# Performance work log

Hardware: AMD Instinct MI355X
Metric: run time of the kernel (lower is better)

Reference implementation:

```python
import jax, jax.numpy as jnp
import numpy as np
import math

B, S, D = 2, 2048, 2048
H = 16
DK = D // H  # 128
DFF = 5440
THETA = 10000.0
EPS = 1e-5


def setup_inputs() -> dict:
    key = jax.random.key(0)
    ks = jax.random.split(key, 9)
    sc = 0.02
    return {
        "x": jax.random.normal(ks[0], (B, S, D), jnp.float32),
        "wq": jax.random.normal(ks[1], (D, D), jnp.float32) * sc,
        "wk": jax.random.normal(ks[2], (D, D), jnp.float32) * sc,
        "wv": jax.random.normal(ks[3], (D, D), jnp.float32) * sc,
        "wo": jax.random.normal(ks[4], (D, D), jnp.float32) * sc,
        "w1": jax.random.normal(ks[5], (DFF, D), jnp.float32) * sc,
        "w2": jax.random.normal(ks[6], (D, DFF), jnp.float32) * sc,
        "w3": jax.random.normal(ks[7], (DFF, D), jnp.float32) * sc,
        "g_attn": jnp.ones((D,), jnp.float32),
        "g_ffn": jnp.ones((D,), jnp.float32),
    }


def _rmsnorm(x, g):
    xf = x.astype(jnp.float32)
    rms = jnp.sqrt(jnp.mean(xf * xf, axis=-1, keepdims=True) + EPS)
    return (xf / rms * g).astype(x.dtype)


def _rope(x):
    # x: (B, H, S, DK)
    pair = jnp.arange(0, DK, 2, dtype=jnp.float32)
    inv_freq = 1.0 / (THETA ** (pair / DK))            # (DK/2,)
    pos = jnp.arange(S, dtype=jnp.float32)
    ang = pos[:, None] * inv_freq[None, :]             # (S, DK/2)
    cos, sin = jnp.cos(ang), jnp.sin(ang)
    xe, xo = x[..., 0::2], x[..., 1::2]
    oe = xe * cos - xo * sin
    oo = xe * sin + xo * cos
    # interleave even/odd back
    out = jnp.stack([oe, oo], axis=-1).reshape(x.shape)
    return out


def reference(x, wq, wk, wv, wo, w1, w2, w3, g_attn, g_ffn):
    # --- attention sublayer ---
    h = _rmsnorm(x, g_attn)
    q = (h @ wq.T).reshape(B, S, H, DK).transpose(0, 2, 1, 3)
    k = (h @ wk.T).reshape(B, S, H, DK).transpose(0, 2, 1, 3)
    v = (h @ wv.T).reshape(B, S, H, DK).transpose(0, 2, 1, 3)
    q = _rope(q)
    k = _rope(k)
    scores = jnp.einsum("bhqd,bhkd->bhqk", q, k) / math.sqrt(DK)
    causal = jnp.tril(jnp.ones((S, S), dtype=bool))
    scores = jnp.where(causal, scores, jnp.finfo(scores.dtype).min)
    attn = jax.nn.softmax(scores, axis=-1)
    o = jnp.einsum("bhqk,bhkd->bhqd", attn, v)
    o = o.transpose(0, 2, 1, 3).reshape(B, S, D)
    x = x + o @ wo.T
    # --- SwiGLU FFN sublayer ---
    h = _rmsnorm(x, g_ffn)
    a = h @ w1.T
    gate = a * jax.nn.sigmoid(a)
    ff = (gate * (h @ w3.T)) @ w2.T
    return x + ff
```

## Files before the change

kernel.cpp:

```cpp
#include <hip/hip_runtime.h>
#include <cstdint>
#include <cstddef>

typedef float  f32x4  __attribute__((ext_vector_type(4)));
typedef __bf16 bf16x8 __attribute__((ext_vector_type(8)));
typedef unsigned short u16x8 __attribute__((ext_vector_type(8)));
typedef unsigned short u16x4 __attribute__((ext_vector_type(4)));
typedef unsigned short u16x2 __attribute__((ext_vector_type(2)));

#define DEV static __device__ __forceinline__

DEV unsigned short f2bfu(float f) { __bf16 b = (__bf16)f; return __builtin_bit_cast(unsigned short, b); }
DEV float bfu2f(unsigned short u) { return (float)__builtin_bit_cast(__bf16, u); }
DEV bf16x8 ldb8(const void* p) { return __builtin_bit_cast(bf16x8, *(const u16x8*)p); }
DEV float fexp(float x) { return __builtin_amdgcn_exp2f(x * 1.44269504f); }

DEV f32x4 mfma16(bf16x8 a, bf16x8 b, f32x4 c) {
  return __builtin_amdgcn_mfma_f32_16x16x32_bf16(a, b, c, 0, 0, 0);
}

DEV void gload16(const void* g, void* l) {
  __builtin_amdgcn_global_load_lds((const unsigned int*)g, (unsigned int*)l, 16, 0, 0);
}

#define FENCE() asm volatile("" ::: "memory")
#define LGKM0() asm volatile("s_waitcnt lgkmcnt(0)" ::: "memory")
#define VMC4()  asm volatile("s_waitcnt vmcnt(4)" ::: "memory")
#define VMC0()  asm volatile("s_waitcnt vmcnt(0)" ::: "memory")

__global__ __launch_bounds__(256) void conv_cat3(
    const float* __restrict__ s0, const float* __restrict__ s1,
    const float* __restrict__ s2, unsigned short* __restrict__ d)
{
  size_t i = (size_t)blockIdx.x * 256 + threadIdx.x;
  size_t e = i * 4;
  const float* s = e < 4194304 ? s0 : (e < 8388608 ? s1 : s2);
  f32x4 v = *(const f32x4*)(s + (e & 4194303));
  u16x4 o = { f2bfu(v.x), f2bfu(v.y), f2bfu(v.z), f2bfu(v.w) };
  *(u16x4*)(d + e) = o;
}

__global__ __launch_bounds__(256) void conv_plain(
    const float* __restrict__ s, unsigned short* __restrict__ d)
{
  size_t e = ((size_t)blockIdx.x * 256 + threadIdx.x) * 4;
  f32x4 v = *(const f32x4*)(s + e);
  u16x4 o = { f2bfu(v.x), f2bfu(v.y), f2bfu(v.z), f2bfu(v.w) };
  *(u16x4*)(d + e) = o;
}

__global__ __launch_bounds__(256) void conv_w13(
    const float* __restrict__ w1, const float* __restrict__ w3,
    unsigned short* __restrict__ d)
{
  size_t i = (size_t)blockIdx.x * 256 + threadIdx.x;
  size_t e = i * 4;
  if (e >= 22544384ull) return;
  int n = (int)(e >> 11), kc = (int)(e & 2047);
  int grp = n >> 4;
  int srcrow = (grp >> 1) * 16 + (n & 15);
  if (srcrow >= 5440) srcrow = 5439;
  const float* s = (grp & 1) ? w3 : w1;
  size_t off = (size_t)srcrow * 2048 + kc;
  f32x4 v = *(const f32x4*)(s + off);
  u16x4 o = { f2bfu(v.x), f2bfu(v.y), f2bfu(v.z), f2bfu(v.w) };
  *(u16x4*)(d + e) = o;
}

template<int EPI>
__global__ __launch_bounds__(256) void gemm_f(
    const unsigned short* __restrict__ A, const unsigned short* __restrict__ B,
    void* __restrict__ D0, void* __restrict__ D1, void* __restrict__ D2,
    const float* __restrict__ auxf, const float* __restrict__ cosT,
    const float* __restrict__ sinT, int M, int N, int K)
{
  __shared__ __align__(16) unsigned short As[128 * 64];
  __shared__ __align__(16) unsigned short Bs[128 * 64];
  const int tid = threadIdx.x, lane = tid & 63, w = tid >> 6;
  const int wr = w >> 1, wc = w & 1, l15 = lane & 15, lg = lane >> 4;
  const int m0 = blockIdx.x * 128, n0 = blockIdx.y * 128;

  const int srow  = tid >> 3;
  const int scol8 = (tid & 7) ^ (srow & 7);
  const unsigned short* Asrc = A + (size_t)(m0 + srow) * K + scol8 * 8;
  const unsigned short* Bsrc = B + (size_t)(n0 + srow) * K + scol8 * 8;

  f32x4 zero = {0.f, 0.f, 0.f, 0.f};
  f32x4 acc[4][4];
#pragma unroll
  for (int i = 0; i < 4; i++)
#pragma unroll
    for (int j = 0; j < 4; j++) acc[i][j] = zero;

  for (int k0 = 0; k0 < K; k0 += 64) {
#pragma unroll
    for (int p = 0; p < 4; ++p) {
      gload16(Asrc + (size_t)(p * 32) * K + k0, As + (p * 256 + w * 64) * 8);
      gload16(Bsrc + (size_t)(p * 32) * K + k0, Bs + (p * 256 + w * 64) * 8);
    }
    __syncthreads();
    bf16x8 af[2][4], bfr[2][4];
#pragma unroll
    for (int kk = 0; kk < 2; ++kk) {
#pragma unroll
      for (int i = 0; i < 4; ++i) {
        int rA = wr * 64 + i * 16 + l15;
        af[kk][i]  = ldb8(As + rA * 64 + ((((kk << 2) | lg)) ^ (rA & 7)) * 8);
        int rB = wc * 64 + i * 16 + l15;
        bfr[kk][i] = ldb8(Bs + rB * 64 + ((((kk << 2) | lg)) ^ (rB & 7)) * 8);
      }
    }
#pragma unroll
    for (int kk = 0; kk < 2; ++kk)
#pragma unroll
      for (int mi = 0; mi < 4; mi++)
#pragma unroll
        for (int ni = 0; ni < 4; ni++)
          acc[mi][ni] = mfma16(af[kk][mi], bfr[kk][ni], acc[mi][ni]);
    __syncthreads();
  }

  if constexpr (EPI == 0) {
    unsigned short* qd = (unsigned short*)D0;
    unsigned short* kd = (unsigned short*)D1;
    unsigned short* vd = (unsigned short*)D2;
#pragma unroll
    for (int mi = 0; mi < 4; mi++) {
#pragma unroll
      for (int ni = 0; ni < 4; ni++) {
        int col = n0 + wc * 64 + ni * 16 + l15;
#pragma unroll
        for (int r = 0; r < 4; r++) {
          int row = m0 + wr * 64 + mi * 16 + lg * 4 + r;
          float v = acc[mi][ni][r];
          if (col < 4096) {
            int d = col & 127, pi = d >> 1, sp = row & 2047;
            float c = cosT[sp * 64 + pi], s = sinT[sp * 64 + pi];
            float part = __shfl_xor(v, 1);
            float res = (d & 1) ? (part * s + v * c) : (v * c - part * s);
            unsigned short* dst = (col < 2048) ? qd : kd;
            dst[(size_t)row * 2048 + (col & 2047)] = f2bfu(res);
          } else {
            int vdc = col - 4096;
            vd[((size_t)((row >> 11) * 2048 + vdc)) * 2048 + (row & 2047)] = f2bfu(v);
          }
        }
      }
    }
  } else {
    float* O = (float*)D0;
#pragma unroll
    for (int mi = 0; mi < 4; mi++)
#pragma unroll
      for (int ni = 0; ni < 4; ni++) {
        int col = n0 + wc * 64 + ni * 16 + l15;
#pragma unroll
        for (int r = 0; r < 4; r++) {
          int row = m0 + wr * 64 + mi * 16 + lg * 4 + r;
          size_t ix = (size_t)row * 2048 + col;
          if constexpr (EPI == 1) O[ix] = auxf[ix] + acc[mi][ni][r];
          else                    O[ix] = O[ix] + acc[mi][ni][r];
        }
      }
  }
}

template<int EPI>
__global__ __launch_bounds__(512, 1) void gemm8(
    const unsigned short* __restrict__ A, const unsigned short* __restrict__ B,
    void* __restrict__ D0, int M, int N, int K)
{
  __shared__ __align__(16) char Asb[3 * 16384];
  __shared__ __align__(16) char Bsb[3 * 16384];

  const int tid = threadIdx.x, lane = tid & 63, w = tid >> 6;
  const int wm = w >> 2, wn = w & 3;
  const int l15 = lane & 15, lg = lane >> 4;

  const int nwg = gridDim.x, chunk = nwg >> 3;
  const int wg = (blockIdx.x & 7) * chunk + (blockIdx.x >> 3);
  const int MT = M >> 8;
  const int mt = wg % MT, nt = wg / MT;
  const int m0 = mt * 256, n0 = nt * 256;

  const int srow0 = tid >> 2, srow1 = 128 + srow0;
  const int s4d = tid & 3;
  const int s4s0 = s4d ^ ((srow0 >> 1) & 3);
  const int s4s1 = s4d ^ ((srow1 >> 1) & 3);
  const size_t aoff0 = (size_t)(m0 + srow0) * K + s4s0 * 8;
  const size_t aoff1 = (size_t)(m0 + srow1) * K + s4s1 * 8;
  const size_t boff0 = (size_t)(n0 + srow0) * K + s4s0 * 8;
  const size_t boff1 = (size_t)(n0 + srow1) * K + s4s1 * 8;
  const int d0b = srow0 * 64 + s4d * 16;
  const int d1b = srow1 * 64 + s4d * 16;

  f32x4 zero = {0.f, 0.f, 0.f, 0.f};
  f32x4 acc[8][4];
#pragma unroll
  for (int i = 0; i < 8; i++)
#pragma unroll
    for (int j = 0; j < 4; j++) acc[i][j] = zero;

  const int nkt = K >> 5;

  gload16(A + aoff0, Asb + d0b);
  gload16(A + aoff1, Asb + d1b);
  gload16(B + boff0, Bsb + d0b);
  gload16(B + boff1, Bsb + d1b);
  gload16(A + aoff0 + 32, Asb + 16384 + d0b);
  gload16(A + aoff1 + 32, Asb + 16384 + d1b);
  gload16(B + boff0 + 32, Bsb + 16384 + d0b);
  gload16(B + boff1 + 32, Bsb + 16384 + d1b);
  VMC4();
  FENCE();
  __builtin_amdgcn_s_barrier();

  int arow[8], aro[8], brow[4], bro[4];
#pragma unroll
  for (int mi = 0; mi < 8; mi++) {
    arow[mi] = wm * 128 + mi * 16 + l15;
    aro[mi] = arow[mi] * 64 + ((lg ^ ((arow[mi] >> 1) & 3)) << 4);
  }
#pragma unroll
  for (int ni = 0; ni < 4; ni++) {
    brow[ni] = wn * 64 + ni * 16 + l15;
    bro[ni] = brow[ni] * 64 + ((lg ^ ((brow[ni] >> 1) & 3)) << 4);
  }

  int cur = 0, nxt = 2;
  for (int t = 0; t < nkt; ++t) {
    const char* As = Asb + cur * 16384;
    const char* Bs = Bsb + cur * 16384;
    const bool pf = (t + 2) < nkt;
    const size_t kpf = (size_t)(t + 2) * 32;
    char* Apf = Asb + nxt * 16384;
    char* Bpf = Bsb + nxt * 16384;

    bf16x8 bf_[4], af_[4];
#pragma unroll
    for (int ni = 0; ni < 4; ni++) bf_[ni] = ldb8(Bs + bro[ni]);
#pragma unroll
    for (int mi = 0; mi < 4; mi++) af_[mi] = ldb8(As + aro[mi]);
    if (pf) {
      gload16(A + aoff0 + kpf, Apf + d0b);
      gload16(A + aoff1 + kpf, Apf + d1b);
    }
    FENCE();
    __builtin_amdgcn_s_barrier();
    LGKM0();
    __builtin_amdgcn_sched_barrier(0);
    __builtin_amdgcn_s_setprio(1);
#pragma unroll
    for (int mi = 0; mi < 4; mi++)
#pragma unroll
      for (int ni = 0; ni < 4; ni++)
        acc[mi][ni] = mfma16(af_[mi], bf_[ni], acc[mi][ni]);
    __builtin_amdgcn_s_setprio(0);
    FENCE();
    __builtin_amdgcn_s_barrier();

    bf16x8 ag_[4];
#pragma unroll
    for (int mi = 0; mi < 4; mi++) ag_[mi] = ldb8(As + aro[mi + 4]);
    if (pf) {
      gload16(B + boff0 + kpf, Bpf + d0b);
      gload16(B + boff1 + kpf, Bpf + d1b);
    }
    FENCE();
    __builtin_amdgcn_s_barrier();
    LGKM0();
    __builtin_amdgcn_sched_barrier(0);
    __builtin_amdgcn_s_setprio(1);
#pragma unroll
    for (int mi = 0; mi < 4; mi++)
#pragma unroll
      for (int ni = 0; ni < 4; ni++)
        acc[mi + 4][ni] = mfma16(ag_[mi], bf_[ni], acc[mi + 4][ni]);
    __builtin_amdgcn_s_setprio(0);
    if (pf) { VMC4(); } else { VMC0(); }
    FENCE();
    __builtin_amdgcn_s_barrier();

    cur = cur == 2 ? 0 : cur + 1;
    nxt = nxt == 2 ? 0 : nxt + 1;
  }

  if constexpr (EPI == 2) {
    unsigned short* G = (unsigned short*)D0;
#pragma unroll
    for (int mi = 0; mi < 8; mi++)
#pragma unroll
      for (int nj = 0; nj < 2; nj++) {
        int outc = (nt * 8 + wn * 2 + nj) * 16 + l15;
        if (outc >= 5440) continue;
#pragma unroll
        for (int r = 0; r < 4; r++) {
          int row = m0 + wm * 128 + mi * 16 + lg * 4 + r;
          float a = acc[mi][2 * nj][r];
          float c = acc[mi][2 * nj + 1][r];
          float sg = a / (1.0f + fexp(-a));
          G[(size_t)row * 5440 + outc] = f2bfu(sg * c);
        }
      }
  }
}

__global__ __launch_bounds__(256) void rmsnorm_k(
    const float* __restrict__ x, const float* __restrict__ g,
    unsigned short* __restrict__ out)
{
  int row = blockIdx.x, t = threadIdx.x;
  const float* xr = x + (size_t)row * 2048;
  f32x4 v0 = ((const f32x4*)xr)[t];
  f32x4 v1 = ((const f32x4*)xr)[t + 256];
  float ss = v0.x*v0.x + v0.y*v0.y + v0.z*v0.z + v0.w*v0.w
           + v1.x*v1.x + v1.y*v1.y + v1.z*v1.z + v1.w*v1.w;
  __shared__ float red[256];
  red[t] = ss; __syncthreads();
  for (int sh = 128; sh > 0; sh >>= 1) {
    if (t < sh) red[t] += red[t + sh];
    __syncthreads();
  }
  float rinv = rsqrtf(red[0] * (1.0f / 2048.0f) + 1e-5f);
  f32x4 g0 = ((const f32x4*)g)[t];
  f32x4 g1 = ((const f32x4*)g)[t + 256];
  u16x4 o0 = { f2bfu(v0.x*rinv*g0.x), f2bfu(v0.y*rinv*g0.y),
               f2bfu(v0.z*rinv*g0.z), f2bfu(v0.w*rinv*g0.w) };
  u16x4 o1 = { f2bfu(v1.x*rinv*g1.x), f2bfu(v1.y*rinv*g1.y),
               f2bfu(v1.z*rinv*g1.z), f2bfu(v1.w*rinv*g1.w) };
  *(u16x4*)(out + (size_t)row * 2048 + t * 4) = o0;
  *(u16x4*)(out + (size_t)row * 2048 + 1024 + t * 4) = o1;
}

__global__ __launch_bounds__(256) void rope_tab(float* __restrict__ cosT,
                                                float* __restrict__ sinT)
{
  int idx = blockIdx.x * 256 + threadIdx.x;
  int s = idx >> 6, p = idx & 63;
  float ang = (float)s * powf(10000.0f, -(float)p / 64.0f);
  cosT[idx] = cosf(ang);
  sinT[idx] = sinf(ang);
}

__global__ __launch_bounds__(256) void attn_fwd(
    const unsigned short* __restrict__ q, const unsigned short* __restrict__ k,
    const unsigned short* __restrict__ vt, unsigned short* __restrict__ o)
{
  const int S = 2048, Dm = 2048;
  const int tid  = threadIdx.x;
  const int lane = tid & 63;
  const int w    = tid >> 6;
  const int hh   = blockIdx.y, b = blockIdx.z;
  const int l15  = lane & 15, lg = lane >> 4;
  const float SCALE = 0.08838834764831845f;

  __shared__ __align__(16) unsigned short Ks[64 * 128];
  __shared__ __align__(16) unsigned short Vs[128 * 64];
  __shared__ __align__(16) unsigned short Ps[4][16 * 76];

  const unsigned short* kg = k  + ((size_t)(b * S)) * Dm + hh * 128;
  const unsigned short* vg = vt + ((size_t)((b * 16 + hh) * 128)) * S;

  for (int half = 0; half < 2; ++half) {
    const int qt = half ? (31 - blockIdx.x) : blockIdx.x;
    const int r0 = qt * 64;
    const int myq = r0 + w * 16 + l15;

    bf16x8 qf[4];
    size_t qbase = ((size_t)(b * S + r0 + w * 16 + l15)) * Dm + hh * 128 + lg * 8;
#pragma unroll
    for (int kk = 0; kk < 4; kk++) qf[kk] = ldb8(q + qbase + kk * 32);

    f32x4 zero = {0.f, 0.f, 0.f, 0.f};
    f32x4 accO[8];
#pragma unroll
    for (int dt = 0; dt < 8; dt++) accO[dt] = zero;
    float mrun = -1e30f, lrun = 0.f;

    int ntile = qt + 1;
    for (int j = 0; j < ntile; ++j) {
      int kv0 = j * 64;
#pragma unroll
      for (int i = 0; i < 4; i++) {
        int idx = i * 256 + tid;
        int row = idx >> 4, slot = idx & 15;
        u16x8 vv = *(const u16x8*)(kg + (size_t)(kv0 + row) * Dm + slot * 8);
        int boff = (row * 256 + slot * 16) ^ ((row & 7) << 4);
        *(u16x8*)((char*)Ks + boff) = vv;
      }
#pragma unroll
      for (int i = 0; i < 4; i++) {
        int idx = i * 256 + tid;
        int row = idx >> 3, slot = idx & 7;
        u16x8 vv = *(const u16x8*)(vg + (size_t)row * S + kv0 + slot * 8);
        int boff = (row * 128 + slot * 16) ^ ((row & 7) << 4);
        *(u16x8*)((char*)Vs + boff) = vv;
      }
      __syncthreads();

      f32x4 sfr[4];
#pragma unroll
      for (int sv = 0; sv < 4; sv++) sfr[sv] = zero;
#pragma unroll
      for (int kk = 0; kk < 4; kk++) {
#pragma unroll
        for (int sv = 0; sv < 4; sv++) {
          int row = sv * 16 + l15;
          int boff = (row * 256 + kk * 64 + lg * 16) ^ ((row & 7) << 4);
          bf16x8 kf = ldb8((const unsigned short*)((const char*)Ks + boff));
          sfr[sv] = mfma16(kf, qf[kk], sfr[sv]);
        }
      }

      float tmax = -1e30f;
#pragma unroll
      for (int sv = 0; sv < 4; sv++)
#pragma unroll
        for (int r = 0; r < 4; r++) {
          int kvv = kv0 + sv * 16 + lg * 4 + r;
          float val = (kvv <= myq) ? sfr[sv][r] * SCALE : -1e30f;
          sfr[sv][r] = val;
          tmax = fmaxf(tmax, val);
        }
      tmax = fmaxf(tmax, __shfl_xor(tmax, 16));
      tmax = fmaxf(tmax, __shfl_xor(tmax, 32));
      float mnew = fmaxf(mrun, tmax);
      float alpha = fexp(mrun - mnew);
      float psum = 0.f;
#pragma unroll
      for (int sv = 0; sv < 4; sv++)
#pragma unroll
        for (int r = 0; r < 4; r++) {
          float pvv = fexp(sfr[sv][r] - mnew);
          sfr[sv][r] = pvv;
          psum += pvv;
        }
      psum += __shfl_xor(psum, 16);
      psum += __shfl_xor(psum, 32);
      lrun = lrun * alpha + psum;
      mrun = mnew;

      float al[4];
#pragma unroll
      for (int r = 0; r < 4; r++)
        al[r] = __shfl(alpha, (lane & 48) + lg * 4 + r);
#pragma unroll
      for (int dt = 0; dt < 8; dt++) {
        f32x4 t = accO[dt];
        t[0] *= al[0]; t[1] *= al[1]; t[2] *= al[2]; t[3] *= al[3];
        accO[dt] = t;
      }

#pragma unroll
      for (int sv = 0; sv < 4; sv++) {
        u16x2 lo = { f2bfu(sfr[sv][0]), f2bfu(sfr[sv][1]) };
        u16x2 hi = { f2bfu(sfr[sv][2]), f2bfu(sfr[sv][3]) };
        *(u16x2*)&Ps[w][l15 * 76 + sv * 16 + lg * 4]     = lo;
        *(u16x2*)&Ps[w][l15 * 76 + sv * 16 + lg * 4 + 2] = hi;
      }

      bf16x8 pa[2];
      pa[0] = ldb8(&Ps[w][l15 * 76 + lg * 8]);
      pa[1] = ldb8(&Ps[w][l15 * 76 + 32 + lg * 8]);
#pragma unroll
      for (int dt = 0; dt < 8; dt++) {
#pragma unroll
        for (int kk = 0; kk < 2; kk++) {
          int row = dt * 16 + l15;
          int boff = (row * 128 + kk * 64 + lg * 16) ^ ((row & 7) << 4);
          bf16x8 vb = ldb8((const unsigned short*)((const char*)Vs + boff));
          accO[dt] = mfma16(pa[kk], vb, accO[dt]);
        }
      }
      __syncthreads();
    }

    float lf[4];
#pragma unroll
    for (int r = 0; r < 4; r++)
      lf[r] = __shfl(lrun, (lane & 48) + lg * 4 + r);
#pragma unroll
    for (int dt = 0; dt < 8; dt++) {
#pragma unroll
      for (int r = 0; r < 4; r++) {
        int qr = r0 + w * 16 + lg * 4 + r;
        o[((size_t)(b * S + qr)) * Dm + hh * 128 + dt * 16 + l15] =
            f2bfu(accO[dt][r] / lf[r]);
      }
    }
  }
}

extern "C" void kernel_launch(void* const* d_in, const int* in_sizes, int n_in,
                              void* d_out, int out_size, void* d_ws, size_t ws_size,
                              hipStream_t stream)
{
  const float* x      = (const float*)d_in[0];
  const float* wq     = (const float*)d_in[1];
  const float* wk     = (const float*)d_in[2];
  const float* wv     = (const float*)d_in[3];
  const float* wo     = (const float*)d_in[4];
  const float* w1     = (const float*)d_in[5];
  const float* w2     = (const float*)d_in[6];
  const float* w3     = (const float*)d_in[7];
  const float* g_attn = (const float*)d_in[8];
  const float* g_ffn  = (const float*)d_in[9];
  float* out = (float*)d_out;

  unsigned short* W = (unsigned short*)d_ws;
  unsigned short* h_bf    = W;
  unsigned short* q_bf    = W + 8388608ull;
  unsigned short* k_bf    = W + 16777216ull;
  unsigned short* vt_bf   = W + 25165824ull;
  unsigned short* o_bf    = W + 33554432ull;
  unsigned short* wqkv_bf = W + 41943040ull;
  unsigned short* wo_bf   = W + 54525952ull;
  unsigned short* w13_bf  = W + 58720256ull;
  unsigned short* w2_bf   = W + 81264640ull;
  unsigned short* a1_bf   = q_bf;
  float* cosT = (float*)o_bf;
  float* sinT = cosT + 131072;

  dim3 blk(256);
  rope_tab<<<512, blk, 0, stream>>>(cosT, sinT);
  conv_cat3<<<12288, blk, 0, stream>>>(wq, wk, wv, wqkv_bf);
  conv_plain<<<4096, blk, 0, stream>>>(wo, wo_bf);
  conv_w13<<<22016, blk, 0, stream>>>(w1, w3, w13_bf);
  conv_plain<<<10880, blk, 0, stream>>>(w2, w2_bf);

  rmsnorm_k<<<4096, blk, 0, stream>>>(x, g_attn, h_bf);

  gemm_f<0><<<dim3(32, 48), blk, 0, stream>>>(h_bf, wqkv_bf, q_bf, k_bf, vt_bf,
                                              nullptr, cosT, sinT, 4096, 6144, 2048);

  attn_fwd<<<dim3(16, 16, 2), blk, 0, stream>>>(q_bf, k_bf, vt_bf, o_bf);

  gemm_f<1><<<dim3(32, 16), blk, 0, stream>>>(o_bf, wo_bf, out, nullptr, nullptr,
                                              x, nullptr, nullptr, 4096, 2048, 2048);
  rmsnorm_k<<<4096, blk, 0, stream>>>(out, g_ffn, h_bf);

  gemm8<2><<<dim3(688), dim3(512), 0, stream>>>(h_bf, w13_bf, a1_bf, 4096, 11008, 2048);

  gemm_f<3><<<dim3(32, 16), blk, 0, stream>>>(a1_bf, w2_bf, out, nullptr, nullptr,
                                              nullptr, nullptr, nullptr, 4096, 2048, 5440);
}
```

Baseline: 726.1 us.

## Double-buffer K-loop in gemm8 and async-prefetch KV tiles in attention

The SwiGLU GEMM now processes 64-wide K steps across two 32-wide half-stages that are double-buffered in 128KB of LDS, with fewer barriers per 32 elements of K. The attention kernel swaps synchronous global-to-register-to-LDS copies of K/V for direct global_load_lds prefetches into double-buffered shared memory, so the next tile loads while the current one is computed. This aims to hide global memory latency and remove register staging, at the cost of more LDS, which may reduce occupancy for attention, and more delicate vmcnt accounting.

New measurement: 698.1 us. 1.04x faster.

```diff
diff --git a/kernel.cpp b/kernel.cpp
--- a/kernel.cpp
+++ b/kernel.cpp
@@ -25,8 +25,13 @@
 
 #define FENCE() asm volatile("" ::: "memory")
 #define LGKM0() asm volatile("s_waitcnt lgkmcnt(0)" ::: "memory")
+#define VMC8()  asm volatile("s_waitcnt vmcnt(8)" ::: "memory")
 #define VMC4()  asm volatile("s_waitcnt vmcnt(4)" ::: "memory")
 #define VMC0()  asm volatile("s_waitcnt vmcnt(0)" ::: "memory")
+#define SBAR()  __builtin_amdgcn_s_barrier()
+#define SCH0()  __builtin_amdgcn_sched_barrier(0)
+#define PRIO1() __builtin_amdgcn_s_setprio(1)
+#define PRIO0() __builtin_amdgcn_s_setprio(0)
 
 __global__ __launch_bounds__(256) void conv_cat3(
     const float* __restrict__ s0, const float* __restrict__ s1,
@@ -166,12 +171,12 @@
 }
 
 template<int EPI>
-__global__ __launch_bounds__(512, 1) void gemm8(
+__global__ __launch_bounds__(512, 1) void gemm8v2(
     const unsigned short* __restrict__ A, const unsigned short* __restrict__ B,
     void* __restrict__ D0, int M, int N, int K)
 {
-  __shared__ __align__(16) char Asb[3 * 16384];
-  __shared__ __align__(16) char Bsb[3 * 16384];
+  __shared__ __align__(16) char Asb[4 * 16384];
+  __shared__ __align__(16) char Bsb[4 * 16384];
 
   const int tid = threadIdx.x, lane = tid & 63, w = tid >> 6;
   const int wm = w >> 2, wn = w & 3;
@@ -183,16 +188,21 @@
   const int mt = wg % MT, nt = wg / MT;
   const int m0 = mt * 256, n0 = nt * 256;
 
-  const int srow0 = tid >> 2, srow1 = 128 + srow0;
-  const int s4d = tid & 3;
-  const int s4s0 = s4d ^ ((srow0 >> 1) & 3);
-  const int s4s1 = s4d ^ ((srow1 >> 1) & 3);
-  const size_t aoff0 = (size_t)(m0 + srow0) * K + s4s0 * 8;
-  const size_t aoff1 = (size_t)(m0 + srow1) * K + s4s1 * 8;
-  const size_t boff0 = (size_t)(n0 + srow0) * K + s4s0 * 8;
-  const size_t boff1 = (size_t)(n0 + srow1) * K + s4s1 * 8;
-  const int d0b = srow0 * 64 + s4d * 16;
-  const int d1b = srow1 * 64 + s4d * 16;
+  const int srow = tid >> 2;
+  const int s4   = tid & 3;
+  const int s4s  = s4 ^ ((srow >> 1) & 3);
+  const unsigned short* As0 = A + (size_t)(m0 + srow) * K + s4s * 8;
+  const unsigned short* As1 = A + (size_t)(m0 + 128 + srow) * K + s4s * 8;
+  const unsigned short* Bs0 = B + (size_t)(n0 + srow) * K + s4s * 8;
+  const unsigned short* Bs1 = B + (size_t)(n0 + 128 + srow) * K + s4s * 8;
+  const int dst0 = tid * 16, dst1 = 8192 + tid * 16;
+
+#define STAGE_A(kh, db, kt) do { char* rgn = Asb + ((kh)*2+(db))*16384;       \
+    gload16(As0 + (size_t)(kt)*64 + (kh)*32, rgn + dst0);                      \
+    gload16(As1 + (size_t)(kt)*64 + (kh)*32, rgn + dst1); } while(0)
+#define STAGE_B(kh, db, kt) do { char* rgn = Bsb + ((kh)*2+(db))*16384;       \
+    gload16(Bs0 + (size_t)(kt)*64 + (kh)*32, rgn + dst0);                      \
+    gload16(Bs1 + (size_t)(kt)*64 + (kh)*32, rgn + dst1); } while(0)
 
   f32x4 zero = {0.f, 0.f, 0.f, 0.f};
   f32x4 acc[8][4];
@@ -201,89 +211,89 @@
 #pragma unroll
     for (int j = 0; j < 4; j++) acc[i][j] = zero;
 
-  const int nkt = K >> 5;
-
-  gload16(A + aoff0, Asb + d0b);
-  gload16(A + aoff1, Asb + d1b);
-  gload16(B + boff0, Bsb + d0b);
-  gload16(B + boff1, Bsb + d1b);
-  gload16(A + aoff0 + 32, Asb + 16384 + d0b);
-  gload16(A + aoff1 + 32, Asb + 16384 + d1b);
-  gload16(B + boff0 + 32, Bsb + 16384 + d0b);
-  gload16(B + boff1 + 32, Bsb + 16384 + d1b);
-  VMC4();
-  FENCE();
-  __builtin_amdgcn_s_barrier();
-
-  int arow[8], aro[8], brow[4], bro[4];
+  int aro[8], bro[4];
 #pragma unroll
   for (int mi = 0; mi < 8; mi++) {
-    arow[mi] = wm * 128 + mi * 16 + l15;
-    aro[mi] = arow[mi] * 64 + ((lg ^ ((arow[mi] >> 1) & 3)) << 4);
+    int row = wm * 128 + mi * 16 + l15;
+    aro[mi] = row * 64 + ((lg ^ ((row >> 1) & 3)) << 4);
   }
 #pragma unroll
   for (int ni = 0; ni < 4; ni++) {
-    brow[ni] = wn * 64 + ni * 16 + l15;
-    bro[ni] = brow[ni] * 64 + ((lg ^ ((brow[ni] >> 1) & 3)) << 4);
-  }
-
-  int cur = 0, nxt = 2;
+    int row = wn * 64 + ni * 16 + l15;
+    bro[ni] = row * 64 + ((lg ^ ((row >> 1) & 3)) << 4);
+  }
+
+  const int nkt = K >> 6;
+
+  STAGE_A(0, 0, 0); STAGE_B(0, 0, 0); STAGE_A(1, 0, 0); STAGE_B(1, 0, 0);
+
   for (int t = 0; t < nkt; ++t) {
-    const char* As = Asb + cur * 16384;
-    const char* Bs = Bsb + cur * 16384;
-    const bool pf = (t + 2) < nkt;
-    const size_t kpf = (size_t)(t + 2) * 32;
-    char* Apf = Asb + nxt * 16384;
-    char* Bpf = Bsb + nxt * 16384;
-
-    bf16x8 bf_[4], af_[4];
-#pragma unroll
-    for (int ni = 0; ni < 4; ni++) bf_[ni] = ldb8(Bs + bro[ni]);
-#pragma unroll
-    for (int mi = 0; mi < 4; mi++) af_[mi] = ldb8(As + aro[mi]);
-    if (pf) {
-      gload16(A + aoff0 + kpf, Apf + d0b);
-      gload16(A + aoff1 + kpf, Apf + d1b);
-    }
-    FENCE();
-    __builtin_amdgcn_s_barrier();
-    LGKM0();
-    __builtin_amdgcn_sched_barrier(0);
-    __builtin_amdgcn_s_setprio(1);
+    const int db = t & 1, dn = db ^ 1;
+    const bool pf = (t + 1) < nkt;
+    const char* Ar0 = Asb + (0 * 2 + db) * 16384;
+    const char* Br0 = Bsb + (0 * 2 + db) * 16384;
+    const char* Ar1 = Asb + (1 * 2 + db) * 16384;
+    const char* Br1 = Bsb + (1 * 2 + db) * 16384;
+
+    VMC4(); FENCE(); SBAR();
+    bf16x8 bfr[4], af[4];
+#pragma unroll
+    for (int ni = 0; ni < 4; ni++) bfr[ni] = ldb8(Br0 + bro[ni]);
+#pragma unroll
+    for (int mi = 0; mi < 4; mi++) af[mi] = ldb8(Ar0 + aro[mi]);
+    if (pf) STAGE_A(0, dn, t + 1);
+    LGKM0(); SCH0();
+    PRIO1();
 #pragma unroll
     for (int mi = 0; mi < 4; mi++)
 #pragma unroll
       for (int ni = 0; ni < 4; ni++)
-        acc[mi][ni] = mfma16(af_[mi], bf_[ni], acc[mi][ni]);
-    __builtin_amdgcn_s_setprio(0);
-    FENCE();
-    __builtin_amdgcn_s_barrier();
-
-    bf16x8 ag_[4];
-#pragma unroll
-    for (int mi = 0; mi < 4; mi++) ag_[mi] = ldb8(As + aro[mi + 4]);
-    if (pf) {
-      gload16(B + boff0 + kpf, Bpf + d0b);
-      gload16(B + boff1 + kpf, Bpf + d1b);
-    }
-    FENCE();
-    __builtin_amdgcn_s_barrier();
-    LGKM0();
-    __builtin_amdgcn_sched_barrier(0);
-    __builtin_amdgcn_s_setprio(1);
+        acc[mi][ni] = mfma16(af[mi], bfr[ni], acc[mi][ni]);
+    PRIO0();
+
+    bf16x8 ag[4];
+#pragma unroll
+    for (int mi = 0; mi < 4; mi++) ag[mi] = ldb8(Ar0 + aro[mi + 4]);
+    if (pf) STAGE_B(0, dn, t + 1);
+    LGKM0(); SCH0();
+    PRIO1();
 #pragma unroll
     for (int mi = 0; mi < 4; mi++)
 #pragma unroll
       for (int ni = 0; ni < 4; ni++)
-        acc[mi + 4][ni] = mfma16(ag_[mi], bf_[ni], acc[mi + 4][ni]);
-    __builtin_amdgcn_s_setprio(0);
+        acc[mi + 4][ni] = mfma16(ag[mi], bfr[ni], acc[mi + 4][ni]);
+    PRIO0();
+
     if (pf) { VMC4(); } else { VMC0(); }
-    FENCE();
-    __builtin_amdgcn_s_barrier();
-
-    cur = cur == 2 ? 0 : cur + 1;
-    nxt = nxt == 2 ? 0 : nxt + 1;
-  }
+    FENCE(); SBAR();
+#pragma unroll
+    for (int ni = 0; ni < 4; ni++) bfr[ni] = ldb8(Br1 + bro[ni]);
+#pragma unroll
+    for (int mi = 0; mi < 4; mi++) af[mi] = ldb8(Ar1 + aro[mi]);
+    if (pf) STAGE_A(1, dn, t + 1);
+    LGKM0(); SCH0();
+    PRIO1();
+#pragma unroll
+    for (int mi = 0; mi < 4; mi++)
+#pragma unroll
+      for (int ni = 0; ni < 4; ni++)
+        acc[mi][ni] = mfma16(af[mi], bfr[ni], acc[mi][ni]);
+    PRIO0();
+
+#pragma unroll
+    for (int mi = 0; mi < 4; mi++) ag[mi] = ldb8(Ar1 + aro[mi + 4]);
+    if (pf) STAGE_B(1, dn, t + 1);
+    LGKM0(); SCH0();
+    PRIO1();
+#pragma unroll
+    for (int mi = 0; mi < 4; mi++)
+#pragma unroll
+      for (int ni = 0; ni < 4; ni++)
+        acc[mi + 4][ni] = mfma16(ag[mi], bfr[ni], acc[mi + 4][ni]);
+    PRIO0();
+  }
+#undef STAGE_A
+#undef STAGE_B
 
   if constexpr (EPI == 2) {
     unsigned short* G = (unsigned short*)D0;
@@ -354,18 +364,35 @@
   const int l15  = lane & 15, lg = lane >> 4;
   const float SCALE = 0.08838834764831845f;
 
-  __shared__ __align__(16) unsigned short Ks[64 * 128];
-  __shared__ __align__(16) unsigned short Vs[128 * 64];
+  __shared__ __align__(16) char Ksb[2][16384];
+  __shared__ __align__(16) char Vsb[2][16384];
   __shared__ __align__(16) unsigned short Ps[4][16 * 76];
 
   const unsigned short* kg = k  + ((size_t)(b * S)) * Dm + hh * 128;
   const unsigned short* vg = vt + ((size_t)((b * 16 + hh) * 128)) * S;
+
+  const int krs = tid >> 4, ksp = (tid & 15) ^ (krs & 7);
+  const int vrs = tid >> 3, vsp = (tid & 7) ^ (vrs & 7);
+
+#define STAGE_KV(j, buf) do {                                                  \
+    int kv_ = (j) * 64;                                                        \
+    _Pragma("unroll")                                                          \
+    for (int rr = 0; rr < 4; rr++)                                             \
+      gload16(kg + (size_t)(kv_ + rr * 16 + krs) * 2048 + ksp * 8,             \
+              Ksb[buf] + (rr * 256 + tid) * 16);                               \
+    _Pragma("unroll")                                                          \
+    for (int rr = 0; rr < 4; rr++)                                             \
+      gload16(vg + (size_t)(rr * 32 + vrs) * 2048 + kv_ + vsp * 8,             \
+              Vsb[buf] + (rr * 256 + tid) * 16);                               \
+  } while (0)
 
   for (int half = 0; half < 2; ++half) {
     const int qt = half ? (31 - blockIdx.x) : blockIdx.x;
     const int r0 = qt * 64;
     const int myq = r0 + w * 16 + l15;
 
+    STAGE_KV(0, 0);
+
     bf16x8 qf[4];
     size_t qbase = ((size_t)(b * S + r0 + w * 16 + l15)) * Dm + hh * 128 + lg * 8;
 #pragma unroll
@@ -380,23 +407,14 @@
     int ntile = qt + 1;
     for (int j = 0; j < ntile; ++j) {
       int kv0 = j * 64;
-#pragma unroll
-      for (int i = 0; i < 4; i++) {
-        int idx = i * 256 + tid;
-        int row = idx >> 4, slot = idx & 15;
-        u16x8 vv = *(const u16x8*)(kg + (size_t)(kv0 + row) * Dm + slot * 8);
-        int boff = (row * 256 + slot * 16) ^ ((row & 7) << 4);
-        *(u16x8*)((char*)Ks + boff) = vv;
-      }
-#pragma unroll
-      for (int i = 0; i < 4; i++) {
-        int idx = i * 256 + tid;
-        int row = idx >> 3, slot = idx & 7;
-        u16x8 vv = *(const u16x8*)(vg + (size_t)row * S + kv0 + slot * 8);
-        int boff = (row * 128 + slot * 16) ^ ((row & 7) << 4);
-        *(u16x8*)((char*)Vs + boff) = vv;
-      }
-      __syncthreads();
+      const int db = j & 1;
+      const bool pf = (j + 1) < ntile;
+      if (pf) STAGE_KV(j + 1, db ^ 1);
+      if (pf) { VMC8(); } else { VMC0(); }
+      FENCE(); SBAR();
+
+      const char* Ks = Ksb[db];
+      const char* Vs = Vsb[db];
 
       f32x4 sfr[4];
 #pragma unroll
@@ -407,7 +425,7 @@
         for (int sv = 0; sv < 4; sv++) {
           int row = sv * 16 + l15;
           int boff = (row * 256 + kk * 64 + lg * 16) ^ ((row & 7) << 4);
-          bf16x8 kf = ldb8((const unsigned short*)((const char*)Ks + boff));
+          bf16x8 kf = ldb8(Ks + boff);
           sfr[sv] = mfma16(kf, qf[kk], sfr[sv]);
         }
       }
@@ -468,11 +486,11 @@
         for (int kk = 0; kk < 2; kk++) {
           int row = dt * 16 + l15;
           int boff = (row * 128 + kk * 64 + lg * 16) ^ ((row & 7) << 4);
-          bf16x8 vb = ldb8((const unsigned short*)((const char*)Vs + boff));
+          bf16x8 vb = ldb8(Vs + boff);
           accO[dt] = mfma16(pa[kk], vb, accO[dt]);
         }
       }
-      __syncthreads();
+      FENCE(); SBAR();
     }
 
     float lf[4];
@@ -489,6 +507,7 @@
       }
     }
   }
+#undef STAGE_KV
 }
 
 extern "C" void kernel_launch(void* const* d_in, const int* in_sizes, int n_in,
@@ -539,7 +558,7 @@
                                               x, nullptr, nullptr, 4096, 2048, 2048);
   rmsnorm_k<<<4096, blk, 0, stream>>>(out, g_ffn, h_bf);
 
-  gemm8<2><<<dim3(688), dim3(512), 0, stream>>>(h_bf, w13_bf, a1_bf, 4096, 11008, 2048);
+  gemm8v2<2><<<dim3(688), dim3(512), 0, stream>>>(h_bf, w13_bf, a1_bf, 4096, 11008, 2048);
 
   gemm_f<3><<<dim3(32, 16), blk, 0, stream>>>(a1_bf, w2_bf, out, nullptr, nullptr,
                                               nullptr, nullptr, nullptr, 4096, 2048, 5440);
```
